# Kernel optimization log

Measured on AMD Instinct MI355X. Metric: run time of the kernel, lower is better.

## Reference

```python
import jax, jax.numpy as jnp
import numpy as np

K, D = 8, 4
LOG2PI = float(np.log(2.0 * np.pi))
TRIL_ROWS, TRIL_COLS = np.tril_indices(D)


def setup_inputs() -> dict:
    key = jax.random.key(0)
    k1, k2 = jax.random.split(key)
    M = 512
    B = 4096
    phi_dim = K + K * D + K * D * (D + 1) // 2  # 120
    phi = jax.random.normal(k1, (M, phi_dim), dtype=jnp.float32)
    X_ref = jax.random.normal(k2, (B, D), dtype=jnp.float32)
    return {"phi": phi, "X_ref": X_ref}


def reference(phi, X_ref):
    M = phi.shape[0]
    B = X_ref.shape[0]
    # unpack_phi: [pi_tilde | mu | L_vecs]
    pi_tilde = phi[:, :K]                                   # [M, K]
    mu = phi[:, K:K + K * D].reshape(M, K, D)               # [M, K, D]
    L_vecs = phi[:, K + K * D:].reshape(M, K, D * (D + 1) // 2)
    # L_vec_to_matrix: lower-triangular fill (row-major tril order)
    L = jnp.zeros((M, K, D, D), phi.dtype).at[:, :, TRIL_ROWS, TRIL_COLS].set(L_vecs)
    pi = jax.nn.softmax(pi_tilde, axis=-1)                  # [M, K]

    # --- mean responsibilities (GMM E-step) ---
    diff = X_ref[None, None, :, :] - mu[:, :, None, :]      # [M, K, B, D]
    L_flat = L.reshape(M * K, D, D)
    diff_flat = jnp.transpose(diff.reshape(M * K, B, D), (0, 2, 1))  # [MK, D, B]
    alpha = jax.scipy.linalg.solve_triangular(L_flat, diff_flat, lower=True)
    maha = (alpha ** 2).sum(1).reshape(M, K, B)             # Mahalanobis distances
    log_det = 2.0 * jnp.log(
        jnp.clip(jnp.abs(jnp.diagonal(L_flat, axis1=-2, axis2=-1)), 1e-8)
    ).sum(-1).reshape(M, K)
    log_norm = -0.5 * (D * LOG2PI + log_det[:, :, None])
    log_gauss = log_norm - 0.5 * maha                       # [M, K, B]
    log_joint = jnp.log(jnp.clip(pi, 1e-8))[:, :, None] + log_gauss
    log_resp = log_joint - jax.scipy.special.logsumexp(log_joint, axis=1, keepdims=True)
    resp = jnp.exp(log_resp).mean(-1)                       # [M, K]

    # --- combined embedding: [mu | log|diag L| | pi | resp] ---
    mu_flat = mu.reshape(M, K * D)
    L_diag = jnp.diagonal(L, axis1=-2, axis2=-1)            # [M, K, D]
    log_L_flat = jnp.log(jnp.clip(jnp.abs(L_diag), 1e-6)).reshape(M, K * D)
    z = jnp.concatenate([mu_flat, log_L_flat, pi, resp], axis=-1)

    # per-feature standardization across particles (torch.std => ddof=1)
    mean = z.mean(axis=0, keepdims=True)
    std = jnp.clip(z.std(axis=0, ddof=1, keepdims=True), 1e-6)
    return (z - mean) / std
```

## Files before the change

### kernel.cpp

```cpp
#include <hip/hip_runtime.h>
#include <math.h>

#define KK 8
#define LOG2E  1.4426950408889634f
#define HL2E   0.7213475204444817f
#define LOG2PI 1.8378770664093453f

__global__ __launch_bounds__(256) void gmm_main(const float* __restrict__ phi,
                                                const float* __restrict__ X,
                                                float* __restrict__ z,
                                                float* __restrict__ ws) {
    __shared__ float4 sp[KK][4];

    const int b = blockIdx.x;
    const int m = b >> 2;
    const int sub = b & 3;
    const int t = threadIdx.x;
    const float* row = phi + m * 120;

    if (t < KK) {
        float mx = row[0];
        #pragma unroll
        for (int j = 1; j < KK; ++j) mx = fmaxf(mx, row[j]);
        float s = 0.f;
        #pragma unroll
        for (int j = 0; j < KK; ++j) s += __expf(row[j] - mx);
        float pik = __expf(row[t] - mx) / s;
        if (sub == 0) z[m * 80 + 64 + t] = pik;

        const float* muk = row + 8 + t * 4;
        const float* Lv  = row + 40 + t * 10;
        float l00 = Lv[0], l10 = Lv[1], l11 = Lv[2], l20 = Lv[3], l21 = Lv[4],
              l22 = Lv[5], l30 = Lv[6], l31 = Lv[7], l32 = Lv[8], l33 = Lv[9];
        float i0 = 1.f / l00, i1 = 1.f / l11, i2 = 1.f / l22, i3 = 1.f / l33;
        float w00 = i0;
        float w10 = -i1 * l10 * w00;
        float w11 = i1;
        float w20 = -i2 * (l20 * w00 + l21 * w10);
        float w21 = -i2 * (l21 * w11);
        float w22 = i2;
        float w30 = -i3 * (l30 * w00 + l31 * w10 + l32 * w20);
        float w31 = -i3 * (l31 * w11 + l32 * w21);
        float w32 = -i3 * (l32 * w22);
        float w33 = i3;
        float logdet = 2.f * (__logf(fmaxf(fabsf(l00), 1e-8f)) +
                              __logf(fmaxf(fabsf(l11), 1e-8f)) +
                              __logf(fmaxf(fabsf(l22), 1e-8f)) +
                              __logf(fmaxf(fabsf(l33), 1e-8f)));
        float c2 = (__logf(fmaxf(pik, 1e-8f)) -
                    0.5f * (4.f * LOG2PI + logdet)) * LOG2E;
        sp[t][0] = make_float4(muk[0], muk[1], muk[2], muk[3]);
        sp[t][1] = make_float4(w00, w10, w11, w20);
        sp[t][2] = make_float4(w21, w22, w30, w31);
        sp[t][3] = make_float4(w32, w33, c2, 0.f);
    } else if (sub == 0 && t >= 64 && t < 96) {
        int j = t - 64;
        z[m * 80 + j] = row[8 + j];
    } else if (sub == 0 && t >= 96 && t < 128) {
        int j = t - 96, k = j >> 2, d = j & 3;
        int didx = (d == 0) ? 0 : (d == 1) ? 2 : (d == 2) ? 5 : 9;
        z[m * 80 + 32 + j] = __logf(fmaxf(fabsf(row[40 + k * 10 + didx]), 1e-6f));
    }
    __syncthreads();

    float acc[KK];
    #pragma unroll
    for (int k = 0; k < KK; ++k) acc[k] = 0.f;

    const float4* X4 = reinterpret_cast<const float4*>(X);
    float4 xv[4];
    #pragma unroll
    for (int i = 0; i < 4; ++i) xv[i] = X4[sub * 1024 + i * 256 + t];

    float lj[4][KK];
    #pragma unroll
    for (int k = 0; k < KK; ++k) {
        float4 p0 = sp[k][0], p1 = sp[k][1], p2 = sp[k][2], p3 = sp[k][3];
        #pragma unroll
        for (int i = 0; i < 4; ++i) {
            float d0 = xv[i].x - p0.x;
            float d1 = xv[i].y - p0.y;
            float d2 = xv[i].z - p0.z;
            float d3 = xv[i].w - p0.w;
            float a0 = d0 * p1.x;
            float a1 = fmaf(p1.y, d0, d1 * p1.z);
            float a2 = fmaf(p1.w, d0, fmaf(p2.x, d1, d2 * p2.y));
            float a3 = fmaf(p2.z, d0, fmaf(p2.w, d1, fmaf(p3.x, d2, d3 * p3.y)));
            float sq = fmaf(a0, a0, fmaf(a1, a1, fmaf(a2, a2, a3 * a3)));
            lj[i][k] = fmaf(-HL2E, sq, p3.z);
        }
    }
    #pragma unroll
    for (int i = 0; i < 4; ++i) {
        float mx = lj[i][0];
        #pragma unroll
        for (int k = 1; k < KK; ++k) mx = fmaxf(mx, lj[i][k]);
        float e[KK], s = 0.f;
        #pragma unroll
        for (int k = 0; k < KK; ++k) {
            e[k] = __builtin_amdgcn_exp2f(lj[i][k] - mx);
            s += e[k];
        }
        float inv = __builtin_amdgcn_rcpf(s);
        #pragma unroll
        for (int k = 0; k < KK; ++k) acc[k] = fmaf(e[k], inv, acc[k]);
    }

    #pragma unroll
    for (int k = 0; k < KK; ++k) {
        float v = acc[k];
        #pragma unroll
        for (int off = 32; off; off >>= 1) v += __shfl_xor(v, off, 64);
        acc[k] = v;
    }
    if ((t & 63) == 0) {
        const int wid = t >> 6;
        float* w = ws + ((size_t)b * 4 + wid) * 8;
        reinterpret_cast<float4*>(w)[0] = make_float4(acc[0], acc[1], acc[2], acc[3]);
        reinterpret_cast<float4*>(w)[1] = make_float4(acc[4], acc[5], acc[6], acc[7]);
    }
}

__global__ __launch_bounds__(512) void gmm_norm(float* __restrict__ z,
                                                const float* __restrict__ ws,
                                                int M) {
    __shared__ float sw[8];
    const int col = blockIdx.x;
    const int t = threadIdx.x;

    float v;
    if (col >= 72) {
        const float* w = ws + (size_t)t * 128 + (col - 72);
        float s = 0.f;
        #pragma unroll
        for (int p = 0; p < 16; ++p) s += w[p * 8];
        v = s;
    } else {
        v = z[t * 80 + col];
    }

    float r = v;
    #pragma unroll
    for (int off = 32; off; off >>= 1) r += __shfl_xor(r, off, 64);
    if ((t & 63) == 0) sw[t >> 6] = r;
    __syncthreads();
    float tot = 0.f;
    #pragma unroll
    for (int w = 0; w < 8; ++w) tot += sw[w];
    float mean = tot / (float)M;
    __syncthreads();

    float d = v - mean;
    r = d * d;
    #pragma unroll
    for (int off = 32; off; off >>= 1) r += __shfl_xor(r, off, 64);
    if ((t & 63) == 0) sw[t >> 6] = r;
    __syncthreads();
    float tot2 = 0.f;
    #pragma unroll
    for (int w = 0; w < 8; ++w) tot2 += sw[w];
    float stdv = fmaxf(sqrtf(tot2 / (float)(M - 1)), 1e-6f);

    z[t * 80 + col] = d / stdv;
}

extern "C" void kernel_launch(void* const* d_in, const int* in_sizes, int n_in,
                              void* d_out, int out_size, void* d_ws, size_t ws_size,
                              hipStream_t stream) {
    const float* phi = (const float*)d_in[0];
    const float* X   = (const float*)d_in[1];
    const int M = in_sizes[0] / 120;
    float* z  = (float*)d_out;
    float* ws = (float*)d_ws;

    gmm_main<<<M * 4, 256, 0, stream>>>(phi, X, z, ws);
    gmm_norm<<<80, 512, 0, stream>>>(z, ws, M);
}
```

Measured before the change: 73.35 us.

## Fold mean and scale into whitening affine map; halve block count per particle

Precomputes a scaled inverse-Cholesky matrix with sqrt(0.5*log2e) folded in, plus a bias vector -W*mu, so each Mahalanobis term becomes a plain affine transform of x followed by negated squares with no per-point subtraction. Each block now processes 2048 points in two chunks instead of 1024, so the grid is halved (M*2 blocks) and the workspace reduction in the norm kernel shrinks to 8 partials. Exact divisions in the per-component setup are replaced with hardware reciprocals. The changes trade fewer arithmetic ops and less per-block setup against lower parallelism, with some small risk to accuracy from the fast reciprocals and the folded bias.

New measurement: 72.01 us. About the same (-1.8%).

```diff
diff --git a/kernel.cpp b/kernel.cpp
--- a/kernel.cpp
+++ b/kernel.cpp
@@ -4,6 +4,7 @@
 #define KK 8
 #define LOG2E  1.4426950408889634f
 #define HL2E   0.7213475204444817f
+#define SQHL2E 0.8493217829f
 #define LOG2PI 1.8378770664093453f
 
 __global__ __launch_bounds__(256) void gmm_main(const float* __restrict__ phi,
@@ -13,8 +14,8 @@
     __shared__ float4 sp[KK][4];
 
     const int b = blockIdx.x;
-    const int m = b >> 2;
-    const int sub = b & 3;
+    const int m = b >> 1;
+    const int sub = b & 1;
     const int t = threadIdx.x;
     const float* row = phi + m * 120;
 
@@ -25,14 +26,17 @@
         float s = 0.f;
         #pragma unroll
         for (int j = 0; j < KK; ++j) s += __expf(row[j] - mx);
-        float pik = __expf(row[t] - mx) / s;
+        float pik = __expf(row[t] - mx) * __builtin_amdgcn_rcpf(s);
         if (sub == 0) z[m * 80 + 64 + t] = pik;
 
         const float* muk = row + 8 + t * 4;
         const float* Lv  = row + 40 + t * 10;
         float l00 = Lv[0], l10 = Lv[1], l11 = Lv[2], l20 = Lv[3], l21 = Lv[4],
               l22 = Lv[5], l30 = Lv[6], l31 = Lv[7], l32 = Lv[8], l33 = Lv[9];
-        float i0 = 1.f / l00, i1 = 1.f / l11, i2 = 1.f / l22, i3 = 1.f / l33;
+        float i0 = __builtin_amdgcn_rcpf(l00);
+        float i1 = __builtin_amdgcn_rcpf(l11);
+        float i2 = __builtin_amdgcn_rcpf(l22);
+        float i3 = __builtin_amdgcn_rcpf(l33);
         float w00 = i0;
         float w10 = -i1 * l10 * w00;
         float w11 = i1;
@@ -43,16 +47,25 @@
         float w31 = -i3 * (l31 * w11 + l32 * w21);
         float w32 = -i3 * (l32 * w22);
         float w33 = i3;
+        float s00 = SQHL2E * w00, s10 = SQHL2E * w10, s11 = SQHL2E * w11,
+              s20 = SQHL2E * w20, s21 = SQHL2E * w21, s22 = SQHL2E * w22,
+              s30 = SQHL2E * w30, s31 = SQHL2E * w31, s32 = SQHL2E * w32,
+              s33 = SQHL2E * w33;
+        float m0 = muk[0], m1 = muk[1], m2 = muk[2], m3 = muk[3];
+        float nv0 = -(s00 * m0);
+        float nv1 = -fmaf(s10, m0, s11 * m1);
+        float nv2 = -fmaf(s20, m0, fmaf(s21, m1, s22 * m2));
+        float nv3 = -fmaf(s30, m0, fmaf(s31, m1, fmaf(s32, m2, s33 * m3)));
         float logdet = 2.f * (__logf(fmaxf(fabsf(l00), 1e-8f)) +
                               __logf(fmaxf(fabsf(l11), 1e-8f)) +
                               __logf(fmaxf(fabsf(l22), 1e-8f)) +
                               __logf(fmaxf(fabsf(l33), 1e-8f)));
         float c2 = (__logf(fmaxf(pik, 1e-8f)) -
                     0.5f * (4.f * LOG2PI + logdet)) * LOG2E;
-        sp[t][0] = make_float4(muk[0], muk[1], muk[2], muk[3]);
-        sp[t][1] = make_float4(w00, w10, w11, w20);
-        sp[t][2] = make_float4(w21, w22, w30, w31);
-        sp[t][3] = make_float4(w32, w33, c2, 0.f);
+        sp[t][0] = make_float4(s00, s10, s11, s20);
+        sp[t][1] = make_float4(s21, s22, s30, s31);
+        sp[t][2] = make_float4(s32, s33, nv0, nv1);
+        sp[t][3] = make_float4(nv2, nv3, c2, 0.f);
     } else if (sub == 0 && t >= 64 && t < 96) {
         int j = t - 64;
         z[m * 80 + j] = row[8 + j];
@@ -68,42 +81,44 @@
     for (int k = 0; k < KK; ++k) acc[k] = 0.f;
 
     const float4* X4 = reinterpret_cast<const float4*>(X);
-    float4 xv[4];
+
     #pragma unroll
-    for (int i = 0; i < 4; ++i) xv[i] = X4[sub * 1024 + i * 256 + t];
+    for (int c = 0; c < 2; ++c) {
+        float4 xv[4];
+        #pragma unroll
+        for (int i = 0; i < 4; ++i) xv[i] = X4[sub * 2048 + c * 1024 + i * 256 + t];
 
-    float lj[4][KK];
-    #pragma unroll
-    for (int k = 0; k < KK; ++k) {
-        float4 p0 = sp[k][0], p1 = sp[k][1], p2 = sp[k][2], p3 = sp[k][3];
+        float lj[4][KK];
+        #pragma unroll
+        for (int k = 0; k < KK; ++k) {
+            float4 p0 = sp[k][0], p1 = sp[k][1], p2 = sp[k][2], p3 = sp[k][3];
+            #pragma unroll
+            for (int i = 0; i < 4; ++i) {
+                float x0 = xv[i].x, x1 = xv[i].y, x2 = xv[i].z, x3 = xv[i].w;
+                float a0 = fmaf(p0.x, x0, p2.z);
+                float a1 = fmaf(p0.y, x0, fmaf(p0.z, x1, p2.w));
+                float a2 = fmaf(p0.w, x0, fmaf(p1.x, x1, fmaf(p1.y, x2, p3.x)));
+                float a3 = fmaf(p1.z, x0, fmaf(p1.w, x1,
+                            fmaf(p2.x, x2, fmaf(p2.y, x3, p3.y))));
+                lj[i][k] = fmaf(-a0, a0, fmaf(-a1, a1,
+                             fmaf(-a2, a2, fmaf(-a3, a3, p3.z))));
+            }
+        }
         #pragma unroll
         for (int i = 0; i < 4; ++i) {
-            float d0 = xv[i].x - p0.x;
-            float d1 = xv[i].y - p0.y;
-            float d2 = xv[i].z - p0.z;
-            float d3 = xv[i].w - p0.w;
-            float a0 = d0 * p1.x;
-            float a1 = fmaf(p1.y, d0, d1 * p1.z);
-            float a2 = fmaf(p1.w, d0, fmaf(p2.x, d1, d2 * p2.y));
-            float a3 = fmaf(p2.z, d0, fmaf(p2.w, d1, fmaf(p3.x, d2, d3 * p3.y)));
-            float sq = fmaf(a0, a0, fmaf(a1, a1, fmaf(a2, a2, a3 * a3)));
-            lj[i][k] = fmaf(-HL2E, sq, p3.z);
+            float mx = lj[i][0];
+            #pragma unroll
+            for (int k = 1; k < KK; ++k) mx = fmaxf(mx, lj[i][k]);
+            float e[KK], s = 0.f;
+            #pragma unroll
+            for (int k = 0; k < KK; ++k) {
+                e[k] = __builtin_amdgcn_exp2f(lj[i][k] - mx);
+                s += e[k];
+            }
+            float inv = __builtin_amdgcn_rcpf(s);
+            #pragma unroll
+            for (int k = 0; k < KK; ++k) acc[k] = fmaf(e[k], inv, acc[k]);
         }
-    }
-    #pragma unroll
-    for (int i = 0; i < 4; ++i) {
-        float mx = lj[i][0];
-        #pragma unroll
-        for (int k = 1; k < KK; ++k) mx = fmaxf(mx, lj[i][k]);
-        float e[KK], s = 0.f;
-        #pragma unroll
-        for (int k = 0; k < KK; ++k) {
-            e[k] = __builtin_amdgcn_exp2f(lj[i][k] - mx);
-            s += e[k];
-        }
-        float inv = __builtin_amdgcn_rcpf(s);
-        #pragma unroll
-        for (int k = 0; k < KK; ++k) acc[k] = fmaf(e[k], inv, acc[k]);
     }
 
     #pragma unroll
@@ -130,10 +145,10 @@
 
     float v;
     if (col >= 72) {
-        const float* w = ws + (size_t)t * 128 + (col - 72);
+        const float* w = ws + (size_t)t * 64 + (col - 72);
         float s = 0.f;
         #pragma unroll
-        for (int p = 0; p < 16; ++p) s += w[p * 8];
+        for (int p = 0; p < 8; ++p) s += w[p * 8];
         v = s;
     } else {
         v = z[t * 80 + col];
@@ -173,6 +188,6 @@
     float* z  = (float*)d_out;
     float* ws = (float*)d_ws;
 
-    gmm_main<<<M * 4, 256, 0, stream>>>(phi, X, z, ws);
+    gmm_main<<<M * 2, 256, 0, stream>>>(phi, X, z, ws);
     gmm_norm<<<80, 512, 0, stream>>>(z, ws, M);
 }
```
